# Performance work log

Measured on AMD Instinct MI355X. Metric: run time of the kernel, lower is better.

## Reference

```python
import jax, jax.numpy as jnp
import numpy as np

DIM = 768
H = 12        # query heads
HKV = 4       # kv heads
G = H // HKV  # GQA group size
HD = 64       # head dim
CAP = 50.0    # soft cap (Gemma-2 style)
EPS = 1e-6
SCALE = HD ** -0.5
B, T, S = 1, 128, 256


def setup_inputs() -> dict:
    key = jax.random.key(0)
    ks = jax.random.split(key, 5)
    s = DIM ** -0.5
    x = jax.random.normal(ks[0], (B, T, S, DIM), jnp.float32)
    Wq = jax.random.normal(ks[1], (DIM, H * HD), jnp.float32) * s
    Wk = jax.random.normal(ks[2], (DIM, HKV * HD), jnp.float32) * s
    Wv = jax.random.normal(ks[3], (DIM, HKV * HD), jnp.float32) * s
    Wo = jax.random.normal(ks[4], (H * HD, DIM), jnp.float32) * s
    q_norm_w = jnp.ones((HD,), jnp.float32)
    k_norm_w = jnp.ones((HD,), jnp.float32)
    return {"x": x, "Wq": Wq, "Wk": Wk, "Wv": Wv, "Wo": Wo,
            "q_norm_w": q_norm_w, "k_norm_w": k_norm_w}


def _rmsnorm(x, w):
    # x: (..., HD)
    return x * jax.lax.rsqrt(jnp.mean(x * x, axis=-1, keepdims=True) + EPS) * w


def reference(x, Wq, Wk, Wv, Wo, q_norm_w, k_norm_w):
    b, t, s, d = x.shape
    n = b * s
    # fold spatial into batch: temporal attention per spatial position
    xf = x.transpose(0, 2, 1, 3).reshape(n, t, d)             # (N, T, D)
    q = (xf @ Wq).reshape(n, t, H, HD).transpose(0, 2, 1, 3)   # (N, H, T, hd)
    k = (xf @ Wk).reshape(n, t, HKV, HD).transpose(0, 2, 1, 3) # (N, Hkv, T, hd)
    v = (xf @ Wv).reshape(n, t, HKV, HD).transpose(0, 2, 1, 3)
    # QKNorm (per-head RMSNorm on head_dim)
    q = _rmsnorm(q, q_norm_w)
    k = _rmsnorm(k, k_norm_w)
    # GQA without materializing repeated K/V: split q heads into (Hkv, G)
    # (repeat_interleave maps query head h -> kv head h // G, matching kv*G+g)
    qg = q.reshape(n, HKV, G, t, HD)
    attn = jnp.einsum('bkgtd,bksd->bkgts', qg, k) * SCALE      # (N, Hkv, G, T, T)
    attn = CAP * jnp.tanh(attn / CAP)                          # soft cap
    causal = jnp.triu(jnp.ones((t, t), bool), 1)               # True above diag
    attn = jnp.where(causal, -jnp.inf, attn)
    attn = jax.nn.softmax(attn, axis=-1)
    out = jnp.einsum('bkgts,bksd->bkgtd', attn, v)             # (N, Hkv, G, T, hd)
    out = out.reshape(n, H, t, HD).transpose(0, 2, 1, 3).reshape(n, t, H * HD)
    out = out @ Wo                                             # (N, T, D)
    return out.reshape(b, s, t, d).transpose(0, 2, 1, 3)        # (B, T, S, D)
```

## Files before the change

kernel.cpp:

```cpp
#include <hip/hip_runtime.h>
#include <stdint.h>
#include <stddef.h>

#define DIM 768
#define NH  12
#define NKV 4
#define HD  64
#define TT  128
#define NS  256

typedef __attribute__((ext_vector_type(8))) short bf16x8;
typedef __attribute__((ext_vector_type(4))) float f32x4;
typedef __attribute__((ext_vector_type(4))) unsigned int u32x4;
typedef __attribute__((ext_vector_type(2))) unsigned int u32x2;

__device__ __forceinline__ unsigned short f2bf(float f) {
  union { float f; unsigned int u; } v; v.f = f;
  return (unsigned short)((v.u + 0x7FFFu + ((v.u >> 16) & 1u)) >> 16);
}

__device__ __forceinline__ void gload_lds16(const void* g, void* l) {
  __builtin_amdgcn_global_load_lds(
      (const __attribute__((address_space(1))) unsigned int*)g,
      (__attribute__((address_space(3))) unsigned int*)l, 16, 0, 0);
}

__global__ __launch_bounds__(256)
void prep_kernel(const float* __restrict__ x, const float* __restrict__ Wq,
                 const float* __restrict__ Wk, const float* __restrict__ Wv,
                 const float* __restrict__ Wo, unsigned short* __restrict__ Wt,
                 unsigned short* __restrict__ WoT, unsigned short* __restrict__ xb) {
  const int b = blockIdx.x, tid = threadIdx.x;
  if (b < 6144) {
    int idx = b * 256 + tid;
    const int n1 = 1280 * DIM;
    if (idx < n1) {
      int c = idx / DIM, kk = idx - c * DIM;
      float v;
      if (c < 768)       v = Wq[kk * 768 + c];
      else if (c < 1024) v = Wk[kk * 256 + (c - 768)];
      else               v = Wv[kk * 256 + (c - 1024)];
      Wt[idx] = f2bf(v);
    } else {
      int i2 = idx - n1;
      int c = i2 / DIM, kk = i2 - c * DIM;
      WoT[i2] = f2bf(Wo[kk * 768 + c]);
    }
  } else {
    int g = (b - 6144) * 256 + tid;
    int r = g / 192;
    int k = g - r * 192;
    int t = r >> 8, n = r & 255;
    f32x4 f = *reinterpret_cast<const f32x4*>(x + (size_t)g * 4);
    u32x2 pk;
    pk[0] = (unsigned)f2bf(f[0]) | ((unsigned)f2bf(f[1]) << 16);
    pk[1] = (unsigned)f2bf(f[2]) | ((unsigned)f2bf(f[3]) << 16);
    *reinterpret_cast<u32x2*>(xb + (size_t)((n << 7) + t) * DIM + k * 4) = pk;
  }
}

__global__ __launch_bounds__(512, 2)
void qkv_kernel(const unsigned short* __restrict__ xb, const float* __restrict__ qnw,
                const float* __restrict__ knw, const unsigned short* __restrict__ Wt,
                unsigned short* __restrict__ qb, unsigned short* __restrict__ kb,
                unsigned short* __restrict__ vTb) {
  extern __shared__ unsigned short lds[];
  const int b = blockIdx.x;
  const int x8 = b & 7, idx = b >> 3;
  const int cbt = idx % 5;
  const int n   = (idx / 5) * 8 + x8;
  const int tid = threadIdx.x;
  const int wave = tid >> 6, lane = tid & 63;
  const int cl = lane & 15, rowg = lane >> 4;
  const int wmw = wave >> 2, wn = wave & 3;
  const int l8 = lane >> 3, s8 = lane & 7;
  const unsigned short* asrc = xb + (size_t)(n * TT + l8) * DIM + (s8 ^ l8) * 8;
  const unsigned short* bsrc = Wt + (size_t)(cbt * 256 + l8) * DIM + (s8 ^ l8) * 8;
  const int swzr = (cl & 7) << 4;
  f32x4 acc[4][4] = {};

#define QKV_STAGE(buf, ko)                                                  \
  {                                                                         \
    unsigned short* Ad = lds + (buf) * 24576;                               \
    unsigned short* Bd = Ad + 8192;                                         \
    _Pragma("unroll")                                                       \
    for (int i = 0; i < 2; ++i) {                                           \
      const int r0 = i * 64 + wave * 8;                                     \
      gload_lds16(asrc + (size_t)r0 * DIM + (ko), Ad + r0 * 64);            \
    }                                                                       \
    _Pragma("unroll")                                                       \
    for (int i = 0; i < 4; ++i) {                                           \
      const int r0 = i * 64 + wave * 8;                                     \
      gload_lds16(bsrc + (size_t)r0 * DIM + (ko), Bd + r0 * 64);            \
    }                                                                       \
  }

  QKV_STAGE(0, 0);
  QKV_STAGE(1, 64);
  #pragma unroll
  for (int kt = 0; kt < 12; ++kt) {
    if (kt < 11) asm volatile("s_waitcnt vmcnt(6)" ::: "memory");
    else         asm volatile("s_waitcnt vmcnt(0)" ::: "memory");
    __builtin_amdgcn_s_barrier();
    __builtin_amdgcn_sched_barrier(0);
    if (kt + 2 < 12) QKV_STAGE((kt + 2) % 3, (kt + 2) * 64);
    const char* Ab = (const char*)(lds + (kt % 3) * 24576);
    const char* Bb = Ab + 16384;
    #pragma unroll
    for (int ks = 0; ks < 2; ++ks) {
      bf16x8 a[4], bb[4];
      #pragma unroll
      for (int m = 0; m < 4; ++m)
        a[m] = *(const bf16x8*)(Ab + (wmw * 64 + m * 16 + cl) * 128 + ((ks * 64 + rowg * 16) ^ swzr));
      #pragma unroll
      for (int nn = 0; nn < 4; ++nn)
        bb[nn] = *(const bf16x8*)(Bb + (wn * 64 + nn * 16 + cl) * 128 + ((ks * 64 + rowg * 16) ^ swzr));
      #pragma unroll
      for (int m = 0; m < 4; ++m)
        #pragma unroll
        for (int nn = 0; nn < 4; ++nn)
          acc[m][nn] = __builtin_amdgcn_mfma_f32_16x16x32_bf16(a[m], bb[nn], acc[m][nn], 0, 0, 0);
    }
  }
#undef QKV_STAGE
  __syncthreads();

  if (cbt == 4) {
    const int kv = wn;
    unsigned short* dst = vTb + (size_t)((n * NKV + kv) * HD) * TT;
    #pragma unroll
    for (int m = 0; m < 4; ++m) {
      const int tb = wmw * 64 + m * 16 + rowg * 4;
      #pragma unroll
      for (int nn = 0; nn < 4; ++nn) {
        const int d = nn * 16 + cl;
        u32x2 pk;
        pk[0] = (unsigned)f2bf(acc[m][nn][0]) | ((unsigned)f2bf(acc[m][nn][1]) << 16);
        pk[1] = (unsigned)f2bf(acc[m][nn][2]) | ((unsigned)f2bf(acc[m][nn][3]) << 16);
        *reinterpret_cast<u32x2*>(dst + (size_t)d * TT + tb) = pk;
      }
    }
  } else {
    const int isq = (cbt < 3);
    const float* nw = isq ? qnw : knw;
    float wfrag[4];
    #pragma unroll
    for (int nn = 0; nn < 4; ++nn) wfrag[nn] = nw[nn * 16 + cl];
    const float rs = isq ? 0.125f : 1.0f;
    #pragma unroll
    for (int m = 0; m < 4; ++m) {
      #pragma unroll
      for (int j = 0; j < 4; ++j) {
        const int t = wmw * 64 + m * 16 + rowg * 4 + j;
        float ss = 0.f;
        #pragma unroll
        for (int nn = 0; nn < 4; ++nn) { float v = acc[m][nn][j]; ss += v * v; }
        #pragma unroll
        for (int dlt = 1; dlt < 16; dlt <<= 1) ss += __shfl_xor(ss, dlt);
        const float r = rsqrtf(ss * (1.f / 64.f) + 1e-6f) * rs;
        #pragma unroll
        for (int nn = 0; nn < 4; ++nn)
          lds[wn * 8192 + t * 64 + nn * 16 + cl] = f2bf(acc[m][nn][j] * r * wfrag[nn]);
      }
    }
    __syncthreads();
    unsigned short* gdst = isq ? qb + ((size_t)n * NH + cbt * 4) * TT * HD
                               : kb + (size_t)n * NKV * TT * HD;
    #pragma unroll
    for (int i = 0; i < 8; ++i) {
      const int c = tid + 512 * i;
      *reinterpret_cast<u32x4*>(gdst + c * 8) = *reinterpret_cast<const u32x4*>(lds + c * 8);
    }
  }
}

__global__ __launch_bounds__(256)
void attn_kernel(const unsigned short* __restrict__ qb, const unsigned short* __restrict__ kb,
                 const unsigned short* __restrict__ vTb, unsigned short* __restrict__ ab) {
  extern __shared__ char smem[];
  unsigned short (*Ks)[72]   = reinterpret_cast<unsigned short (*)[72]>(smem);
  unsigned short (*Vts)[136] = reinterpret_cast<unsigned short (*)[136]>(smem + 18432);
  unsigned short (*Pl)[136]  = reinterpret_cast<unsigned short (*)[136]>(smem + 35840);
  const int b = blockIdx.x;
  const int x8 = b & 7, idx = b >> 3;
  const int kv = idx & 3;
  const int n  = (idx >> 2) * 8 + x8;
  const int tid = threadIdx.x, wave = tid >> 6, lane = tid & 63;
  const int cl = lane & 15, rowg = lane >> 4;

  const unsigned short* ksrc = kb + (size_t)(n * NKV + kv) * TT * HD;
  const unsigned short* vsrc = vTb + (size_t)(n * NKV + kv) * HD * TT;
  #pragma unroll
  for (int i = 0; i < 4; ++i) {
    int c = tid + 256 * i, r = c >> 3, seg = c & 7;
    *reinterpret_cast<u32x4*>(&Ks[r][seg * 8]) = *reinterpret_cast<const u32x4*>(ksrc + c * 8);
  }
  #pragma unroll
  for (int i = 0; i < 4; ++i) {
    int c = tid + 256 * i, r = c >> 4, seg = c & 15;
    *reinterpret_cast<u32x4*>(&Vts[r][seg * 8]) = *reinterpret_cast<const u32x4*>(vsrc + c * 8);
  }
  __syncthreads();

  for (int hh = 0; hh < 3; ++hh) {
    const int h = kv * 3 + hh;
    const unsigned short* qsrc = qb + (size_t)(n * NH + h) * TT * HD;
    f32x4 sc[2][8] = {};
    #pragma unroll
    for (int ks = 0; ks < 2; ++ks) {
      bf16x8 a[2], bbf[8];
      #pragma unroll
      for (int m = 0; m < 2; ++m)
        a[m] = *reinterpret_cast<const bf16x8*>(
            qsrc + (size_t)(wave * 32 + m * 16 + cl) * HD + ks * 32 + rowg * 8);
      #pragma unroll
      for (int nn = 0; nn < 8; ++nn)
        bbf[nn] = *reinterpret_cast<const bf16x8*>(&Ks[nn * 16 + cl][ks * 32 + rowg * 8]);
      #pragma unroll
      for (int m = 0; m < 2; ++m)
        #pragma unroll
        for (int nn = 0; nn < 8; ++nn)
          sc[m][nn] = __builtin_amdgcn_mfma_f32_16x16x32_bf16(a[m], bbf[nn], sc[m][nn], 0, 0, 0);
    }
    #pragma unroll
    for (int m = 0; m < 2; ++m) {
      #pragma unroll
      for (int j = 0; j < 4; ++j) {
        const int rowv = wave * 32 + m * 16 + rowg * 4 + j;
        float mx = -__builtin_inff();
        #pragma unroll
        for (int nn = 0; nn < 8; ++nn) {
          float s = sc[m][nn][j];
          float e = __expf(s * 0.04f);
          s = 50.f - 100.f * __builtin_amdgcn_rcpf(e + 1.f);
          if (nn * 16 + cl > rowv) s = -__builtin_inff();
          sc[m][nn][j] = s;
          mx = fmaxf(mx, s);
        }
        #pragma unroll
        for (int d = 1; d < 16; d <<= 1) mx = fmaxf(mx, __shfl_xor(mx, d));
        float sum = 0.f;
        #pragma unroll
        for (int nn = 0; nn < 8; ++nn) {
          float e = __expf(sc[m][nn][j] - mx);
          sc[m][nn][j] = e;
          sum += e;
        }
        #pragma unroll
        for (int d = 1; d < 16; d <<= 1) sum += __shfl_xor(sum, d);
        const float inv = __builtin_amdgcn_rcpf(sum);
        #pragma unroll
        for (int nn = 0; nn < 8; ++nn)
          Pl[rowv][nn * 16 + cl] = f2bf(sc[m][nn][j] * inv);
      }
    }
    __syncthreads();
    f32x4 o[2][4] = {};
    #pragma unroll
    for (int ks = 0; ks < 4; ++ks) {
      bf16x8 a[2], bbf[4];
      #pragma unroll
      for (int m = 0; m < 2; ++m)
        a[m] = *reinterpret_cast<const bf16x8*>(&Pl[wave * 32 + m * 16 + cl][ks * 32 + rowg * 8]);
      #pragma unroll
      for (int nn = 0; nn < 4; ++nn)
        bbf[nn] = *reinterpret_cast<const bf16x8*>(&Vts[nn * 16 + cl][ks * 32 + rowg * 8]);
      #pragma unroll
      for (int m = 0; m < 2; ++m)
        #pragma unroll
        for (int nn = 0; nn < 4; ++nn)
          o[m][nn] = __builtin_amdgcn_mfma_f32_16x16x32_bf16(a[m], bbf[nn], o[m][nn], 0, 0, 0);
    }
    unsigned short* dst = ab + (size_t)n * TT * DIM + h * HD;
    #pragma unroll
    for (int m = 0; m < 2; ++m)
      #pragma unroll
      for (int j = 0; j < 4; ++j) {
        int t = wave * 32 + m * 16 + rowg * 4 + j;
        #pragma unroll
        for (int nn = 0; nn < 4; ++nn)
          dst[(size_t)t * DIM + nn * 16 + cl] = f2bf(o[m][nn][j]);
      }
    __syncthreads();
  }
}

__global__ __launch_bounds__(512, 2)
void out_kernel(const unsigned short* __restrict__ ab, const unsigned short* __restrict__ WoT,
                float* __restrict__ out) {
  extern __shared__ unsigned short lds[];
  const int b = blockIdx.x;
  const int x8 = b & 7, idx = b >> 3;
  const int cbt = idx % 3;
  const int n   = (idx / 3) * 8 + x8;
  const int tid = threadIdx.x;
  const int wave = tid >> 6, lane = tid & 63;
  const int cl = lane & 15, rowg = lane >> 4;
  const int wmw = wave >> 2, wn = wave & 3;
  const int l8 = lane >> 3, s8 = lane & 7;
  const unsigned short* asrc = ab  + (size_t)(n * TT + l8) * DIM + (s8 ^ l8) * 8;
  const unsigned short* bsrc = WoT + (size_t)(cbt * 256 + l8) * DIM + (s8 ^ l8) * 8;
  const int swzr = (cl & 7) << 4;
  f32x4 acc[4][4] = {};

#define OUT_STAGE(buf, ko)                                                  \
  {                                                                         \
    unsigned short* Ad = lds + (buf) * 24576;                               \
    unsigned short* Bd = Ad + 8192;                                         \
    _Pragma("unroll")                                                       \
    for (int i = 0; i < 2; ++i) {                                           \
      const int r0 = i * 64 + wave * 8;                                     \
      gload_lds16(asrc + (size_t)r0 * DIM + (ko), Ad + r0 * 64);            \
    }                                                                       \
    _Pragma("unroll")                                                       \
    for (int i = 0; i < 4; ++i) {                                           \
      const int r0 = i * 64 + wave * 8;                                     \
      gload_lds16(bsrc + (size_t)r0 * DIM + (ko), Bd + r0 * 64);            \
    }                                                                       \
  }

  OUT_STAGE(0, 0);
  OUT_STAGE(1, 64);
  #pragma unroll
  for (int kt = 0; kt < 12; ++kt) {
    if (kt < 11) asm volatile("s_waitcnt vmcnt(6)" ::: "memory");
    else         asm volatile("s_waitcnt vmcnt(0)" ::: "memory");
    __builtin_amdgcn_s_barrier();
    __builtin_amdgcn_sched_barrier(0);
    if (kt + 2 < 12) OUT_STAGE((kt + 2) % 3, (kt + 2) * 64);
    const char* Ab = (const char*)(lds + (kt % 3) * 24576);
    const char* Bb = Ab + 16384;
    #pragma unroll
    for (int ks = 0; ks < 2; ++ks) {
      bf16x8 a[4], bb[4];
      #pragma unroll
      for (int m = 0; m < 4; ++m)
        a[m] = *(const bf16x8*)(Ab + (wmw * 64 + m * 16 + cl) * 128 + ((ks * 64 + rowg * 16) ^ swzr));
      #pragma unroll
      for (int nn = 0; nn < 4; ++nn)
        bb[nn] = *(const bf16x8*)(Bb + (wn * 64 + nn * 16 + cl) * 128 + ((ks * 64 + rowg * 16) ^ swzr));
      #pragma unroll
      for (int m = 0; m < 4; ++m)
        #pragma unroll
        for (int nn = 0; nn < 4; ++nn)
          acc[m][nn] = __builtin_amdgcn_mfma_f32_16x16x32_bf16(a[m], bb[nn], acc[m][nn], 0, 0, 0);
    }
  }
#undef OUT_STAGE
  #pragma unroll
  for (int m = 0; m < 4; ++m)
    #pragma unroll
    for (int j = 0; j < 4; ++j) {
      int t = wmw * 64 + m * 16 + rowg * 4 + j;
      #pragma unroll
      for (int nn = 0; nn < 4; ++nn)
        out[(size_t)(t * NS + n) * DIM + cbt * 256 + wn * 64 + nn * 16 + cl] = acc[m][nn][j];
    }
}

extern "C" void kernel_launch(void* const* d_in, const int* in_sizes, int n_in,
                              void* d_out, int out_size, void* d_ws, size_t ws_size,
                              hipStream_t stream) {
  const float* x   = (const float*)d_in[0];
  const float* Wq  = (const float*)d_in[1];
  const float* Wk  = (const float*)d_in[2];
  const float* Wv  = (const float*)d_in[3];
  const float* Wo  = (const float*)d_in[4];
  const float* qnw = (const float*)d_in[5];
  const float* knw = (const float*)d_in[6];
  (void)in_sizes; (void)n_in; (void)out_size;

  char* ws = (char*)d_ws;
  unsigned short* Wt  = (unsigned short*)(ws + 0);
  unsigned short* WoT = (unsigned short*)(ws + 1966080);
  unsigned short* qb  = (unsigned short*)(ws + 3145728);
  unsigned short* kb  = (unsigned short*)(ws + 53477376);
  unsigned short* vTb = (unsigned short*)(ws + 70254592);
  unsigned short* ab  = (unsigned short*)(ws + 87031808);
  unsigned short* xb  = ab;
  if (ws_size < 137363456) return;

  hipFuncSetAttribute(reinterpret_cast<const void*>(qkv_kernel),
                      hipFuncAttributeMaxDynamicSharedMemorySize, 147456);
  hipFuncSetAttribute(reinterpret_cast<const void*>(out_kernel),
                      hipFuncAttributeMaxDynamicSharedMemorySize, 147456);
  hipFuncSetAttribute(reinterpret_cast<const void*>(attn_kernel),
                      hipFuncAttributeMaxDynamicSharedMemorySize, 70656);

  prep_kernel<<<30720, 256, 0, stream>>>(x, Wq, Wk, Wv, Wo, Wt, WoT, xb);
  qkv_kernel<<<1280, 512, 147456, stream>>>(xb, qnw, knw, Wt, qb, kb, vTb);
  attn_kernel<<<1024, 256, 70656, stream>>>(qb, kb, vTb, ab);
  out_kernel<<<768, 512, 147456, stream>>>(ab, WoT, (float*)d_out);
}
```

Measured before the change: 223.2 us.

## Restructure GEMM k-loops into four-phase interleaved load/MFMA schedule with setprio

Replaces the QKV and output-projection GEMM main loops with a shared macro that splits each k-tile into four phases. Each phase issues a slice of LDS fragment reads and a slice of the next tile's global-to-LDS loads, then runs 8 MFMAs under raised wave priority. The aim is to spread memory issue across the compute and keep the matrix units fed. In exchange it adds many more barriers per k-tile and uses fewer live A fragments, which could add sync overhead.

```diff
diff --git a/kernel.cpp b/kernel.cpp
--- a/kernel.cpp
+++ b/kernel.cpp
@@ -59,6 +59,76 @@
   }
 }
 
+
+#define STAGE_A(bufp, ko)                                                    \
+  { unsigned short* Ad = lds + (bufp) * 24576;                               \
+    gload_lds16(asrc + (size_t)(wave * 8) * DIM + (ko), Ad + (wave * 8) * 64);\
+    gload_lds16(asrc + (size_t)(64 + wave * 8) * DIM + (ko), Ad + (64 + wave * 8) * 64); }
+#define STAGE_B01(bufp, ko)                                                  \
+  { unsigned short* Bd = lds + (bufp) * 24576 + 8192;                        \
+    gload_lds16(bsrc + (size_t)(wave * 8) * DIM + (ko), Bd + (wave * 8) * 64);\
+    gload_lds16(bsrc + (size_t)(64 + wave * 8) * DIM + (ko), Bd + (64 + wave * 8) * 64); }
+#define STAGE_B23(bufp, ko)                                                  \
+  { unsigned short* Bd = lds + (bufp) * 24576 + 8192;                        \
+    gload_lds16(bsrc + (size_t)(128 + wave * 8) * DIM + (ko), Bd + (128 + wave * 8) * 64);\
+    gload_lds16(bsrc + (size_t)(192 + wave * 8) * DIM + (ko), Bd + (192 + wave * 8) * 64); }
+
+#define LDA(ks, m) (*(const bf16x8*)(Ab + (wmw * 64 + (m) * 16 + cl) * 128 + (((ks) * 64 + rowg * 16) ^ swzr)))
+#define LDB(ks, n) (*(const bf16x8*)(Bb + (wn * 64 + (n) * 16 + cl) * 128 + (((ks) * 64 + rowg * 16) ^ swzr)))
+
+#define MFMA8(mlo, av0, av1)                                                 \
+  __builtin_amdgcn_s_setprio(1);                                             \
+  _Pragma("unroll")                                                          \
+  for (int nn = 0; nn < 4; ++nn) {                                           \
+    acc[(mlo)][nn]     = __builtin_amdgcn_mfma_f32_16x16x32_bf16(av0, bb[nn], acc[(mlo)][nn], 0, 0, 0);     \
+    acc[(mlo) + 1][nn] = __builtin_amdgcn_mfma_f32_16x16x32_bf16(av1, bb[nn], acc[(mlo) + 1][nn], 0, 0, 0); \
+  }                                                                          \
+  __builtin_amdgcn_s_setprio(0);
+
+#define KLOOP_8PHASE                                                         \
+  STAGE_A(0, 0); STAGE_B01(0, 0); STAGE_B23(0, 0);                           \
+  STAGE_A(1, 64); STAGE_B01(1, 64); STAGE_B23(1, 64);                        \
+  asm volatile("s_waitcnt vmcnt(6)" ::: "memory");                           \
+  __builtin_amdgcn_s_barrier();                                              \
+  _Pragma("unroll")                                                          \
+  for (int kt = 0; kt < 12; ++kt) {                                          \
+    const char* Ab = (const char*)(lds + (kt % 3) * 24576);                  \
+    const char* Bb = Ab + 16384;                                             \
+    const int bufn = (kt + 2) % 3; const int kon = (kt + 2) * 64;            \
+    bf16x8 a0, a1, bb[4];                                                    \
+                                                     \
+    a0 = LDA(0, 0); a1 = LDA(0, 1);                                          \
+    bb[0] = LDB(0, 0); bb[1] = LDB(0, 1); bb[2] = LDB(0, 2); bb[3] = LDB(0, 3);\
+    if (kt < 10) STAGE_A(bufn, kon);                                         \
+    __builtin_amdgcn_s_barrier();                                            \
+    asm volatile("s_waitcnt lgkmcnt(0)" ::: "memory");                       \
+    MFMA8(0, a0, a1);                                                        \
+    __builtin_amdgcn_s_barrier();                                            \
+                                                     \
+    a0 = LDA(0, 2); a1 = LDA(0, 3);                                          \
+    if (kt < 10) STAGE_B01(bufn, kon);                                       \
+    __builtin_amdgcn_s_barrier();                                            \
+    asm volatile("s_waitcnt lgkmcnt(0)" ::: "memory");                       \
+    MFMA8(2, a0, a1);                                                        \
+    __builtin_amdgcn_s_barrier();                                            \
+                                                     \
+    a0 = LDA(1, 0); a1 = LDA(1, 1);                                          \
+    bb[0] = LDB(1, 0); bb[1] = LDB(1, 1); bb[2] = LDB(1, 2); bb[3] = LDB(1, 3);\
+    if (kt < 10) STAGE_B23(bufn, kon);                                       \
+    __builtin_amdgcn_s_barrier();                                            \
+    asm volatile("s_waitcnt lgkmcnt(0)" ::: "memory");                       \
+    MFMA8(0, a0, a1);                                                        \
+    __builtin_amdgcn_s_barrier();                                            \
+                                    \
+    a0 = LDA(1, 2); a1 = LDA(1, 3);                                          \
+    if (kt <= 9) { asm volatile("s_waitcnt vmcnt(6)" ::: "memory"); }        \
+    else         { asm volatile("s_waitcnt vmcnt(0)" ::: "memory"); }        \
+    __builtin_amdgcn_s_barrier();                                            \
+    asm volatile("s_waitcnt lgkmcnt(0)" ::: "memory");                       \
+    MFMA8(2, a0, a1);                                                        \
+    __builtin_amdgcn_s_barrier();                                            \
+  }
+
 __global__ __launch_bounds__(512, 2)
 void qkv_kernel(const unsigned short* __restrict__ xb, const float* __restrict__ qnw,
                 const float* __restrict__ knw, const unsigned short* __restrict__ Wt,
@@ -79,50 +149,8 @@
   const int swzr = (cl & 7) << 4;
   f32x4 acc[4][4] = {};
 
-#define QKV_STAGE(buf, ko)                                                  \
-  {                                                                         \
-    unsigned short* Ad = lds + (buf) * 24576;                               \
-    unsigned short* Bd = Ad + 8192;                                         \
-    _Pragma("unroll")                                                       \
-    for (int i = 0; i < 2; ++i) {                                           \
-      const int r0 = i * 64 + wave * 8;                                     \
-      gload_lds16(asrc + (size_t)r0 * DIM + (ko), Ad + r0 * 64);            \
-    }                                                                       \
-    _Pragma("unroll")                                                       \
-    for (int i = 0; i < 4; ++i) {                                           \
-      const int r0 = i * 64 + wave * 8;                                     \
-      gload_lds16(bsrc + (size_t)r0 * DIM + (ko), Bd + r0 * 64);            \
-    }                                                                       \
-  }
-
-  QKV_STAGE(0, 0);
-  QKV_STAGE(1, 64);
-  #pragma unroll
-  for (int kt = 0; kt < 12; ++kt) {
-    if (kt < 11) asm volatile("s_waitcnt vmcnt(6)" ::: "memory");
-    else         asm volatile("s_waitcnt vmcnt(0)" ::: "memory");
-    __builtin_amdgcn_s_barrier();
-    __builtin_amdgcn_sched_barrier(0);
-    if (kt + 2 < 12) QKV_STAGE((kt + 2) % 3, (kt + 2) * 64);
-    const char* Ab = (const char*)(lds + (kt % 3) * 24576);
-    const char* Bb = Ab + 16384;
-    #pragma unroll
-    for (int ks = 0; ks < 2; ++ks) {
-      bf16x8 a[4], bb[4];
-      #pragma unroll
-      for (int m = 0; m < 4; ++m)
-        a[m] = *(const bf16x8*)(Ab + (wmw * 64 + m * 16 + cl) * 128 + ((ks * 64 + rowg * 16) ^ swzr));
-      #pragma unroll
-      for (int nn = 0; nn < 4; ++nn)
-        bb[nn] = *(const bf16x8*)(Bb + (wn * 64 + nn * 16 + cl) * 128 + ((ks * 64 + rowg * 16) ^ swzr));
-      #pragma unroll
-      for (int m = 0; m < 4; ++m)
-        #pragma unroll
-        for (int nn = 0; nn < 4; ++nn)
-          acc[m][nn] = __builtin_amdgcn_mfma_f32_16x16x32_bf16(a[m], bb[nn], acc[m][nn], 0, 0, 0);
-    }
-  }
-#undef QKV_STAGE
+  KLOOP_8PHASE;
+
   __syncthreads();
 
   if (cbt == 4) {
@@ -303,50 +331,8 @@
   const int swzr = (cl & 7) << 4;
   f32x4 acc[4][4] = {};
 
-#define OUT_STAGE(buf, ko)                                                  \
-  {                                                                         \
-    unsigned short* Ad = lds + (buf) * 24576;                               \
-    unsigned short* Bd = Ad + 8192;                                         \
-    _Pragma("unroll")                                                       \
-    for (int i = 0; i < 2; ++i) {                                           \
-      const int r0 = i * 64 + wave * 8;                                     \
-      gload_lds16(asrc + (size_t)r0 * DIM + (ko), Ad + r0 * 64);            \
-    }                                                                       \
-    _Pragma("unroll")                                                       \
-    for (int i = 0; i < 4; ++i) {                                           \
-      const int r0 = i * 64 + wave * 8;                                     \
-      gload_lds16(bsrc + (size_t)r0 * DIM + (ko), Bd + r0 * 64);            \
-    }                                                                       \
-  }
-
-  OUT_STAGE(0, 0);
-  OUT_STAGE(1, 64);
-  #pragma unroll
-  for (int kt = 0; kt < 12; ++kt) {
-    if (kt < 11) asm volatile("s_waitcnt vmcnt(6)" ::: "memory");
-    else         asm volatile("s_waitcnt vmcnt(0)" ::: "memory");
-    __builtin_amdgcn_s_barrier();
-    __builtin_amdgcn_sched_barrier(0);
-    if (kt + 2 < 12) OUT_STAGE((kt + 2) % 3, (kt + 2) * 64);
-    const char* Ab = (const char*)(lds + (kt % 3) * 24576);
-    const char* Bb = Ab + 16384;
-    #pragma unroll
-    for (int ks = 0; ks < 2; ++ks) {
-      bf16x8 a[4], bb[4];
-      #pragma unroll
-      for (int m = 0; m < 4; ++m)
-        a[m] = *(const bf16x8*)(Ab + (wmw * 64 + m * 16 + cl) * 128 + ((ks * 64 + rowg * 16) ^ swzr));
-      #pragma unroll
-      for (int nn = 0; nn < 4; ++nn)
-        bb[nn] = *(const bf16x8*)(Bb + (wn * 64 + nn * 16 + cl) * 128 + ((ks * 64 + rowg * 16) ^ swzr));
-      #pragma unroll
-      for (int m = 0; m < 4; ++m)
-        #pragma unroll
-        for (int nn = 0; nn < 4; ++nn)
-          acc[m][nn] = __builtin_amdgcn_mfma_f32_16x16x32_bf16(a[m], bb[nn], acc[m][nn], 0, 0, 0);
-    }
-  }
-#undef OUT_STAGE
+  KLOOP_8PHASE;
+
   #pragma unroll
   for (int m = 0; m < 4; ++m)
     #pragma unroll
```

Result: no change. 225.5 us (+1.0%).
